# Optimization experiments

Hardware: AMD Instinct MI355X
Metric: run time of the kernel (lower is better)

## Reference

```python
import jax, jax.numpy as jnp
import numpy as np

# model geometry (matches init_kwargs cfg)
D = 768        # D_EMB
PATCH = 16
T = 8192
N = T // PATCH # 512 patch tokens
H = 12         # heads
HD = D // H    # 64 head dim
NL = 6         # layers
DFF = 4 * D
B = 8
LN_EPS = 1e-5


def setup_inputs() -> dict:
    key = jax.random.key(0)
    ks = iter(jax.random.split(key, 32))
    def g(shape, scale=0.02):
        return jax.random.normal(next(ks), shape, jnp.float32) * scale
    return dict(
        x=jax.random.normal(next(ks), (B, T), jnp.float32),
        pp_w=g((D, PATCH)), pp_b=jnp.zeros((D,), jnp.float32),
        pe=g((N, D)),
        ln1_g=jnp.ones((NL, D), jnp.float32), ln1_b=jnp.zeros((NL, D), jnp.float32),
        qkv_w=g((NL, 3 * D, D)), out_w=g((NL, D, D)),
        ln2_g=jnp.ones((NL, D), jnp.float32), ln2_b=jnp.zeros((NL, D), jnp.float32),
        fc1_w=g((NL, DFF, D)), fc2_w=g((NL, D, DFF)),
        lnf_g=jnp.ones((D,), jnp.float32), lnf_b=jnp.zeros((D,), jnp.float32),
        h1_w=g((D // 2, D)), h1_b=jnp.zeros((D // 2,), jnp.float32),
        h2_w=g((2, D // 2)), h2_b=jnp.zeros((2,), jnp.float32),
    )


def _ln(x, g, b):
    m = x.mean(-1, keepdims=True)
    v = ((x - m) ** 2).mean(-1, keepdims=True)
    return (x - m) / jnp.sqrt(v + LN_EPS) * g + b


def reference(x, pp_w, pp_b, pe, ln1_g, ln1_b, qkv_w, out_w,
              ln2_g, ln2_b, fc1_w, fc2_w, lnf_g, lnf_b,
              h1_w, h1_b, h2_w, h2_b):
    Bx = x.shape[0]
    # patch embed: [B, N, PATCH] @ W^T + b -> [B, N, D]
    z = jnp.einsum('bnp,dp->bnd', x[:, :N * PATCH].reshape(Bx, N, PATCH), pp_w) + pp_b
    z = z + pe  # positional embedding (arange indexes whole table)
    mask = jnp.tril(jnp.ones((N, N), dtype=bool))
    for i in range(NL):
        # --- attention (manual causal softmax, dropout=eval/no-op) ---
        h = _ln(z, ln1_g[i], ln1_b[i])
        qkv = jnp.einsum('bnd,ed->bne', h, qkv_w[i])            # [B,N,3D]
        qkv = qkv.reshape(Bx, N, 3, H, HD).transpose(2, 0, 3, 1, 4)
        q, k, v = qkv[0], qkv[1], qkv[2]                         # [B,H,N,HD]
        s = jnp.einsum('bhld,bhmd->bhlm', q, k) / np.sqrt(HD)
        s = jnp.where(mask, s, -jnp.inf)
        a = jax.nn.softmax(s, axis=-1)
        o = jnp.einsum('bhlm,bhmd->bhld', a, v)
        o = o.transpose(0, 2, 1, 3).reshape(Bx, N, D)
        z = z + jnp.einsum('bnd,ed->bne', o, out_w[i])
        # --- FFN (exact gelu, matching F.gelu default) ---
        h = _ln(z, ln2_g[i], ln2_b[i])
        f = jax.nn.gelu(jnp.einsum('bnd,fd->bnf', h, fc1_w[i]), approximate=False)
        z = z + jnp.einsum('bnf,df->bnd', f, fc2_w[i])
    enc = _ln(z, lnf_g, lnf_b).mean(axis=1)                      # [B, D]
    y = jax.nn.relu(enc @ h1_w.T + h1_b)
    return y @ h2_w.T + h2_b                                     # [B, 2]
```

## Files before the change

kernel.cpp:

```cpp
#include <hip/hip_runtime.h>
#include <hip/hip_bf16.h>
#include <math.h>

#define D_EMB 768
#define NPATCH 16
#define NTOK 512
#define NHEAD 12
#define HDIM 64
#define NLAYER 6
#define DFF 3072
#define BATCH 8
#define MTOK (BATCH * NTOK)

typedef __attribute__((ext_vector_type(8))) short bf16x8;
typedef __attribute__((ext_vector_type(4))) float f32x4;

__device__ __forceinline__ float bf2f(ushort s) {
    unsigned u = ((unsigned)s) << 16;
    return __builtin_bit_cast(float, u);
}
__device__ __forceinline__ ushort f2bf(float f) {
    unsigned u = __builtin_bit_cast(unsigned, f);
    unsigned r = (u + 0x7FFFu + ((u >> 16) & 1u)) >> 16;
    return (ushort)r;
}

__global__ __launch_bounds__(256)
void f2bf4_kernel(const float* __restrict__ s0, ushort* __restrict__ d0, int n0,
                  const float* __restrict__ s1, ushort* __restrict__ d1, int n1,
                  const float* __restrict__ s2, ushort* __restrict__ d2, int n2,
                  const float* __restrict__ s3, ushort* __restrict__ d3, int n3)
{
    int i = blockIdx.x * 256 + threadIdx.x;
    const float* s; ushort* d; int off;
    if (i < n0)                { s = s0; d = d0; off = i; }
    else if (i < n0 + n1)      { s = s1; d = d1; off = i - n0; }
    else if (i < n0 + n1 + n2) { s = s2; d = d2; off = i - n0 - n1; }
    else if (i < n0 + n1 + n2 + n3) { s = s3; d = d3; off = i - n0 - n1 - n2; }
    else return;
    float4 v = *(const float4*)(s + (size_t)off * 4);
    ushort4 o;
    o.x = f2bf(v.x); o.y = f2bf(v.y); o.z = f2bf(v.z); o.w = f2bf(v.w);
    *(ushort4*)(d + (size_t)off * 4) = o;
}

__global__ __launch_bounds__(256)
void patch_embed_kernel(const float* __restrict__ x, const float* __restrict__ pw,
                        const float* __restrict__ pb, const float* __restrict__ pe,
                        float* __restrict__ z)
{
    int bn = blockIdx.x;
    int b = bn >> 9, n = bn & 511;
    __shared__ float xs[NPATCH];
    int t = threadIdx.x;
    if (t < NPATCH) xs[t] = x[(size_t)b * 8192 + n * NPATCH + t];
    __syncthreads();
    for (int d = t; d < D_EMB; d += 256) {
        float acc = pb[d] + pe[(size_t)n * D_EMB + d];
        const float* w = pw + (size_t)d * NPATCH;
        #pragma unroll
        for (int p = 0; p < NPATCH; ++p) acc += xs[p] * w[p];
        z[(size_t)bn * D_EMB + d] = acc;
    }
}

__device__ __forceinline__ float block_reduce_sum_256(float v)
{
    __shared__ float lds[4];
    #pragma unroll
    for (int o = 32; o > 0; o >>= 1) v += __shfl_xor(v, o);
    int lane = threadIdx.x & 63, wid = threadIdx.x >> 6;
    __syncthreads();
    if (lane == 0) lds[wid] = v;
    __syncthreads();
    return lds[0] + lds[1] + lds[2] + lds[3];
}

__device__ __forceinline__ void store_val(float* p, float v)  { *p = v; }
__device__ __forceinline__ void store_val(ushort* p, float v) { *p = f2bf(v); }

template<typename OT>
__global__ __launch_bounds__(256)
void ln_kernel(const float* __restrict__ x, const float* __restrict__ g,
               const float* __restrict__ bta, OT* __restrict__ y)
{
    int row = blockIdx.x;
    const float* xr = x + (size_t)row * D_EMB;
    int t = threadIdx.x;
    float vals[3];
    float s = 0.f;
    #pragma unroll
    for (int i = 0; i < 3; ++i) { vals[i] = xr[t + i * 256]; s += vals[i]; }
    float mean = block_reduce_sum_256(s) * (1.0f / D_EMB);
    float ss = 0.f;
    #pragma unroll
    for (int i = 0; i < 3; ++i) { float d = vals[i] - mean; ss += d * d; }
    float var = block_reduce_sum_256(ss) * (1.0f / D_EMB);
    float rstd = rsqrtf(var + 1e-5f);
    #pragma unroll
    for (int i = 0; i < 3; ++i) {
        int d = t + i * 256;
        store_val(y + (size_t)row * D_EMB + d, (vals[i] - mean) * rstd * g[d] + bta[d]);
    }
}

#define STAGE64(buf, k0)                                                           \
    {                                                                              \
        _Pragma("unroll")                                                          \
        for (int j = 0; j < 2; ++j) {                                              \
            int row = j * 32 + srow;                                               \
            int lcol = pcol ^ (row & 7);                                           \
            const ushort* sa = Ab + (size_t)(bm + row) * lda + (k0) + (lcol << 3); \
            __builtin_amdgcn_global_load_lds(                                      \
                (const __attribute__((address_space(1))) unsigned int*)sa,         \
                (__attribute__((address_space(3))) unsigned int*)&As[buf][row * 64 + (pcol << 3)], \
                16, 0, 0);                                                         \
        }                                                                          \
        _Pragma("unroll")                                                          \
        for (int j = 0; j < 4; ++j) {                                              \
            int row = j * 32 + srow;                                               \
            int lcol = pcol ^ (row & 7);                                           \
            const ushort* sb = Wb + (size_t)(bn + row) * lda + (k0) + (lcol << 3); \
            __builtin_amdgcn_global_load_lds(                                      \
                (const __attribute__((address_space(1))) unsigned int*)sb,         \
                (__attribute__((address_space(3))) unsigned int*)&Bs[buf][row * 64 + (pcol << 3)], \
                16, 0, 0);                                                         \
        }                                                                          \
    }

#define COMPUTE64(buf)                                                             \
    {                                                                              \
        _Pragma("unroll")                                                          \
        for (int kk = 0; kk < 64; kk += 32) {                                      \
            int c = (kk >> 3) + lg;                                                \
            bf16x8 a[4], b[2];                                                     \
            _Pragma("unroll")                                                      \
            for (int m = 0; m < 4; ++m) {                                          \
                int row = m * 16 + lr;                                             \
                a[m] = *(const bf16x8*)(&As[buf][row * 64 + ((c ^ (row & 7)) << 3)]); \
            }                                                                      \
            _Pragma("unroll")                                                      \
            for (int n = 0; n < 2; ++n) {                                          \
                int row = w * 32 + n * 16 + lr;                                    \
                b[n] = *(const bf16x8*)(&Bs[buf][row * 64 + ((c ^ (row & 7)) << 3)]); \
            }                                                                      \
            _Pragma("unroll")                                                      \
            for (int m = 0; m < 4; ++m) {                                          \
                _Pragma("unroll")                                                  \
                for (int n = 0; n < 2; ++n)                                        \
                    acc[m][n] = __builtin_amdgcn_mfma_f32_16x16x32_bf16(a[m], b[n], acc[m][n], 0, 0, 0); \
            }                                                                      \
        }                                                                          \
    }

template<int EPI, typename OT, bool SPLITK>
__global__ __launch_bounds__(256)
void mfma_gemm(const ushort* __restrict__ A,
               const ushort* __restrict__ W,
               OT* __restrict__ C,
               const float* __restrict__ res,
               int N, int K, int lda)
{
    __shared__ ushort As[2][64 * 64];
    __shared__ ushort Bs[2][128 * 64];

    int gx = gridDim.x, gy = gridDim.y;
    int bx = blockIdx.x, by = blockIdx.y;
    int bz = SPLITK ? blockIdx.z : 0;
    if ((gy & 7) == 0) {
        int flat = bx + gx * (by + gy * bz);
        int xcd = flat & 7, j = flat >> 3;
        int ry = gy >> 3;
        by = xcd * ry + (j % ry);
        int rem = j / ry;
        bx = rem % gx;
        bz = rem / gx;
    }
    int bm = by * 64, bn = bx * 128;

    const ushort* Ab = A + (size_t)bz * K;
    const ushort* Wb = W + (size_t)bz * K;
    OT* Cb = C + (SPLITK ? (size_t)bz * ((size_t)gy * 64) * N : 0);

    int tid = threadIdx.x;
    int w = tid >> 6, l = tid & 63;
    int lr = l & 15, lg = l >> 4;
    f32x4 acc[4][2] = {};

    int srow = w * 8 + (l >> 3);
    int pcol = l & 7;

    const int nk = K >> 6;
    STAGE64(0, 0);
    __syncthreads();
    int cur = 0;
    for (int t = 0; t < nk; ++t) {
        if (t + 1 < nk) STAGE64(cur ^ 1, (t + 1) << 6);
        COMPUTE64(cur);
        __syncthreads();
        cur ^= 1;
    }

    int r0 = lg * 4;
    #pragma unroll
    for (int m = 0; m < 4; ++m) {
        #pragma unroll
        for (int n = 0; n < 2; ++n) {
            #pragma unroll
            for (int j = 0; j < 4; ++j) {
                int gm = bm + m * 16 + r0 + j;
                int gn = bn + w * 32 + n * 16 + lr;
                float v = acc[m][n][j];
                if (EPI == 1) v = 0.5f * v * (1.0f + erff(v * 0.70710678118654752f));
                if (EPI == 2) v += res[(size_t)gm * N + gn];
                store_val(Cb + (size_t)gm * N + gn, v);
            }
        }
    }
}

__global__ __launch_bounds__(256)
void splitk_reduce(const float* __restrict__ p, float* __restrict__ z, int n4)
{
    int i = blockIdx.x * 256 + threadIdx.x;
    if (i >= n4) return;
    float4 a = ((const float4*)p)[i];
    float4 b = ((const float4*)p)[i + (size_t)n4];
    float4 c = ((float4*)z)[i];
    c.x += a.x + b.x; c.y += a.y + b.y; c.z += a.z + b.z; c.w += a.w + b.w;
    ((float4*)z)[i] = c;
}

__global__ __launch_bounds__(256)
void attn_mfma_kernel(const ushort* __restrict__ qkv, ushort* __restrict__ o)
{
    int w = threadIdx.x >> 6, l = threadIdx.x & 63;
    int qt = blockIdx.x * 4 + w;
    int h = blockIdx.y, b = blockIdx.z;
    int q0 = qt * 16;
    int lr = l & 15, lg = l >> 4;

    const size_t rs = 3 * D_EMB;
    const ushort* qbase = qkv + ((size_t)(b * NTOK)) * rs + h * HDIM;
    const ushort* kbase = qbase + D_EMB;
    const ushort* vbase = qbase + 2 * D_EMB;

    bf16x8 qf[2];
    qf[0] = *(const bf16x8*)(qbase + (size_t)(q0 + lr) * rs + lg * 8);
    qf[1] = *(const bf16x8*)(qbase + (size_t)(q0 + lr) * rs + 32 + lg * 8);

    f32x4 oacc[4] = {};
    float m_j[4], l_j[4];
    #pragma unroll
    for (int j = 0; j < 4; ++j) { m_j[j] = -1e30f; l_j[j] = 0.f; }

    __shared__ ushort P_lds[4][16][40];

    int ntiles = q0 / 32 + 1;
    for (int mt = 0; mt < ntiles; ++mt) {
        int m0 = mt * 32;
        f32x4 s[2] = {};
        #pragma unroll
        for (int kb = 0; kb < 2; ++kb) {
            const ushort* kr = kbase + (size_t)(m0 + kb * 16 + lr) * rs;
            bf16x8 k0 = *(const bf16x8*)(kr + lg * 8);
            bf16x8 k1 = *(const bf16x8*)(kr + 32 + lg * 8);
            s[kb] = __builtin_amdgcn_mfma_f32_16x16x32_bf16(qf[0], k0, s[kb], 0, 0, 0);
            s[kb] = __builtin_amdgcn_mfma_f32_16x16x32_bf16(qf[1], k1, s[kb], 0, 0, 0);
        }
        bool partial = (m0 + 31 > q0);
        float p[2][4], mx[4];
        #pragma unroll
        for (int j = 0; j < 4; ++j) {
            int qr = q0 + lg * 4 + j;
            float s0 = s[0][j] * 0.125f;
            float s1 = s[1][j] * 0.125f;
            if (partial) {
                if (m0 + lr > qr)      s0 = -1e30f;
                if (m0 + 16 + lr > qr) s1 = -1e30f;
            }
            p[0][j] = s0; p[1][j] = s1;
            float mm = fmaxf(s0, s1);
            mm = fmaxf(mm, __shfl_xor(mm, 1));
            mm = fmaxf(mm, __shfl_xor(mm, 2));
            mm = fmaxf(mm, __shfl_xor(mm, 4));
            mm = fmaxf(mm, __shfl_xor(mm, 8));
            mx[j] = mm;
        }
        #pragma unroll
        for (int j = 0; j < 4; ++j) {
            float mnew = fmaxf(m_j[j], mx[j]);
            float scale = __expf(m_j[j] - mnew);
            float p0 = __expf(p[0][j] - mnew);
            float p1 = __expf(p[1][j] - mnew);
            p[0][j] = p0; p[1][j] = p1;
            float rsum = p0 + p1;
            rsum += __shfl_xor(rsum, 1);
            rsum += __shfl_xor(rsum, 2);
            rsum += __shfl_xor(rsum, 4);
            rsum += __shfl_xor(rsum, 8);
            l_j[j] = l_j[j] * scale + rsum;
            m_j[j] = mnew;
            #pragma unroll
            for (int i = 0; i < 4; ++i) oacc[i][j] *= scale;
        }
        #pragma unroll
        for (int kb = 0; kb < 2; ++kb)
            #pragma unroll
            for (int j = 0; j < 4; ++j)
                P_lds[w][lg * 4 + j][kb * 16 + lr] = f2bf(p[kb][j]);
        asm volatile("s_waitcnt lgkmcnt(0)" ::: "memory");
        bf16x8 pa = *(const bf16x8*)(&P_lds[w][lr][lg * 8]);
        #pragma unroll
        for (int i = 0; i < 4; ++i) {
            bf16x8 vf;
            const ushort* vp = vbase + (size_t)(m0 + lg * 8) * rs + i * 16 + lr;
            #pragma unroll
            for (int j = 0; j < 8; ++j) vf[j] = (short)vp[(size_t)j * rs];
            oacc[i] = __builtin_amdgcn_mfma_f32_16x16x32_bf16(pa, vf, oacc[i], 0, 0, 0);
        }
    }
    #pragma unroll
    for (int i = 0; i < 4; ++i) {
        #pragma unroll
        for (int j = 0; j < 4; ++j) {
            int qr = q0 + lg * 4 + j;
            int d  = i * 16 + lr;
            float v = oacc[i][j] / l_j[j];
            o[((size_t)(b * NTOK + qr)) * D_EMB + h * HDIM + d] = f2bf(v);
        }
    }
}

__global__ void mean_kernel(const float* __restrict__ x, float* __restrict__ enc)
{
    int b = blockIdx.x; int d = threadIdx.x;
    float s = 0.f;
    for (int n = 0; n < NTOK; ++n) s += x[((size_t)(b * NTOK + n)) * D_EMB + d];
    enc[b * D_EMB + d] = s * (1.0f / NTOK);
}

__global__ void head1_kernel(const float* __restrict__ enc, const float* __restrict__ w,
                             const float* __restrict__ bias, float* __restrict__ r)
{
    int b = blockIdx.x; int j = threadIdx.x;
    float acc = bias[j];
    const float* e = enc + b * D_EMB;
    const float* wr = w + (size_t)j * D_EMB;
    for (int k = 0; k < D_EMB; ++k) acc += e[k] * wr[k];
    r[b * 384 + j] = fmaxf(acc, 0.f);
}

__global__ void head2_kernel(const float* __restrict__ r, const float* __restrict__ w,
                             const float* __restrict__ bias, float* __restrict__ out)
{
    int idx = threadIdx.x;
    if (idx >= 16) return;
    int b = idx >> 1, j = idx & 1;
    float acc = bias[j];
    for (int k = 0; k < 384; ++k) acc += r[b * 384 + k] * w[j * 384 + k];
    out[b * 2 + j] = acc;
}

extern "C" void kernel_launch(void* const* d_in, const int* in_sizes, int n_in,
                              void* d_out, int out_size, void* d_ws, size_t ws_size,
                              hipStream_t stream)
{
    const float* x     = (const float*)d_in[0];
    const float* pp_w  = (const float*)d_in[1];
    const float* pp_b  = (const float*)d_in[2];
    const float* pe    = (const float*)d_in[3];
    const float* ln1_g = (const float*)d_in[4];
    const float* ln1_b = (const float*)d_in[5];
    const float* qkv_w = (const float*)d_in[6];
    const float* out_w = (const float*)d_in[7];
    const float* ln2_g = (const float*)d_in[8];
    const float* ln2_b = (const float*)d_in[9];
    const float* fc1_w = (const float*)d_in[10];
    const float* fc2_w = (const float*)d_in[11];
    const float* lnf_g = (const float*)d_in[12];
    const float* lnf_b = (const float*)d_in[13];
    const float* h1_w  = (const float*)d_in[14];
    const float* h1_b  = (const float*)d_in[15];
    const float* h2_w  = (const float*)d_in[16];
    const float* h2_b  = (const float*)d_in[17];
    float* out = (float*)d_out;

    char* p = (char*)d_ws;
    float*  z      = (float*)p;  p += (size_t)MTOK * D_EMB * 4;
    ushort* big_bf = (ushort*)p; p += (size_t)MTOK * DFF * 2;
    ushort* h_bf   = (ushort*)p; p += (size_t)MTOK * D_EMB * 2;
    ushort* wq_bf  = (ushort*)p; p += (size_t)3 * D_EMB * D_EMB * 2;
    ushort* wo_bf  = (ushort*)p; p += (size_t)D_EMB * D_EMB * 2;
    ushort* wf1_bf = (ushort*)p; p += (size_t)DFF * D_EMB * 2;
    ushort* wf2_bf = (ushort*)p; p += (size_t)D_EMB * DFF * 2;
    float*  pbuf   = (float*)p;  p += (size_t)2 * MTOK * D_EMB * 4;
    float*  enc    = (float*)p;  p += BATCH * D_EMB * 4;
    float*  r1     = (float*)p;  p += BATCH * 384 * 4;
    float*  lnf_out = (float*)big_bf;

    patch_embed_kernel<<<MTOK, 256, 0, stream>>>(x, pp_w, pp_b, pe, z);

    const int nq = 3 * D_EMB * D_EMB, no = D_EMB * D_EMB, nf = DFF * D_EMB;
    const int n4q = nq / 4, n4o = no / 4, n4f = nf / 4;
    const int cvt_blocks = (n4q + n4o + 2 * n4f + 255) / 256;
    const int n4red = MTOK * D_EMB / 4;

    for (int i = 0; i < NLAYER; ++i) {
        f2bf4_kernel<<<cvt_blocks, 256, 0, stream>>>(
            qkv_w + (size_t)i * nq, wq_bf,  n4q,
            out_w + (size_t)i * no, wo_bf,  n4o,
            fc1_w + (size_t)i * nf, wf1_bf, n4f,
            fc2_w + (size_t)i * nf, wf2_bf, n4f);

        ln_kernel<ushort><<<MTOK, 256, 0, stream>>>(z, ln1_g + i * D_EMB, ln1_b + i * D_EMB, h_bf);

        dim3 gq((3 * D_EMB) / 128, MTOK / 64);
        mfma_gemm<0, ushort, false><<<gq, 256, 0, stream>>>(h_bf, wq_bf, big_bf, nullptr,
                                                            3 * D_EMB, D_EMB, D_EMB);

        dim3 ga(NTOK / 64, NHEAD, BATCH);
        attn_mfma_kernel<<<ga, 256, 0, stream>>>(big_bf, h_bf);

        dim3 gp(D_EMB / 128, MTOK / 64);
        mfma_gemm<2, float, false><<<gp, 256, 0, stream>>>(h_bf, wo_bf, z, z,
                                                           D_EMB, D_EMB, D_EMB);

        ln_kernel<ushort><<<MTOK, 256, 0, stream>>>(z, ln2_g + i * D_EMB, ln2_b + i * D_EMB, h_bf);

        dim3 g1(DFF / 128, MTOK / 64);
        mfma_gemm<1, ushort, false><<<g1, 256, 0, stream>>>(h_bf, wf1_bf, big_bf, nullptr,
                                                            DFF, D_EMB, D_EMB);

        dim3 g2(D_EMB / 128, MTOK / 64, 2);
        mfma_gemm<0, float, true><<<g2, 256, 0, stream>>>(big_bf, wf2_bf, pbuf, nullptr,
                                                          D_EMB, DFF / 2, DFF);
        splitk_reduce<<<(n4red + 255) / 256, 256, 0, stream>>>(pbuf, z, n4red);
    }

    ln_kernel<float><<<MTOK, 256, 0, stream>>>(z, lnf_g, lnf_b, lnf_out);
    mean_kernel<<<BATCH, D_EMB, 0, stream>>>(lnf_out, enc);
    head1_kernel<<<BATCH, 384, 0, stream>>>(enc, h1_w, h1_b, r1);
    head2_kernel<<<1, 64, 0, stream>>>(r1, h2_w, h2_b, out);
}
```

Baseline: 1.110 ms.

## Triple-buffer GEMM pipeline, stage attention V via LDS, fuse split-K reduce with LayerNorm

Moves the GEMM from double to triple buffering, with vmcnt-based waits and a single barrier per K-step so loads run two tiles ahead of the MFMAs. The attention kernel now stages each V tile into LDS with async global-to-LDS loads instead of doing strided global reads per element. The split-K reduction is merged with the next layer's LayerNorm (or the final LN), which removes a kernel launch and one full pass over z. The trade-offs are more shared memory per GEMM block, which can lower occupancy, and hand-written waitcnt counts that must match the exact number of issued loads.

```diff
diff --git a/kernel.cpp b/kernel.cpp
--- a/kernel.cpp
+++ b/kernel.cpp
@@ -91,6 +91,40 @@
     float s = 0.f;
     #pragma unroll
     for (int i = 0; i < 3; ++i) { vals[i] = xr[t + i * 256]; s += vals[i]; }
+    float mean = block_reduce_sum_256(s) * (1.0f / D_EMB);
+    float ss = 0.f;
+    #pragma unroll
+    for (int i = 0; i < 3; ++i) { float d = vals[i] - mean; ss += d * d; }
+    float var = block_reduce_sum_256(ss) * (1.0f / D_EMB);
+    float rstd = rsqrtf(var + 1e-5f);
+    #pragma unroll
+    for (int i = 0; i < 3; ++i) {
+        int d = t + i * 256;
+        store_val(y + (size_t)row * D_EMB + d, (vals[i] - mean) * rstd * g[d] + bta[d]);
+    }
+}
+
+template<typename OT>
+__global__ __launch_bounds__(256)
+void reduce_ln_kernel(const float* __restrict__ pbuf, float* __restrict__ z,
+                      const float* __restrict__ g, const float* __restrict__ bta,
+                      OT* __restrict__ y)
+{
+    int row = blockIdx.x;
+    int t = threadIdx.x;
+    const float* p0 = pbuf + (size_t)row * D_EMB;
+    const float* p1 = pbuf + (size_t)MTOK * D_EMB + (size_t)row * D_EMB;
+    float* zr = z + (size_t)row * D_EMB;
+    float vals[3];
+    float s = 0.f;
+    #pragma unroll
+    for (int i = 0; i < 3; ++i) {
+        int d = t + i * 256;
+        float v = zr[d] + p0[d] + p1[d];
+        vals[i] = v;
+        zr[d] = v;
+        s += v;
+    }
     float mean = block_reduce_sum_256(s) * (1.0f / D_EMB);
     float ss = 0.f;
     #pragma unroll
@@ -131,8 +165,8 @@
 #define COMPUTE64(buf)                                                             \
     {                                                                              \
         _Pragma("unroll")                                                          \
-        for (int kk = 0; kk < 64; kk += 32) {                                      \
-            int c = (kk >> 3) + lg;                                                \
+        for (int kk = 0; kk < 2; ++kk) {                                           \
+            int c = kk * 4 + lg;                                                   \
             bf16x8 a[4], b[2];                                                     \
             _Pragma("unroll")                                                      \
             for (int m = 0; m < 4; ++m) {                                          \
@@ -155,14 +189,12 @@
 
 template<int EPI, typename OT, bool SPLITK>
 __global__ __launch_bounds__(256)
-void mfma_gemm(const ushort* __restrict__ A,
-               const ushort* __restrict__ W,
-               OT* __restrict__ C,
-               const float* __restrict__ res,
+void mfma_gemm(const ushort* __restrict__ A, const ushort* __restrict__ W,
+               OT* __restrict__ C, const float* __restrict__ res,
                int N, int K, int lda)
 {
-    __shared__ ushort As[2][64 * 64];
-    __shared__ ushort Bs[2][128 * 64];
+    __shared__ ushort As[3][64 * 64];
+    __shared__ ushort Bs[3][128 * 64];
 
     int gx = gridDim.x, gy = gridDim.y;
     int bx = blockIdx.x, by = blockIdx.y;
@@ -192,13 +224,16 @@
 
     const int nk = K >> 6;
     STAGE64(0, 0);
-    __syncthreads();
-    int cur = 0;
+    STAGE64(1, 64);
     for (int t = 0; t < nk; ++t) {
-        if (t + 1 < nk) STAGE64(cur ^ 1, (t + 1) << 6);
-        COMPUTE64(cur);
-        __syncthreads();
-        cur ^= 1;
+        if (t < nk - 1) { asm volatile("s_waitcnt vmcnt(6)" ::: "memory"); }
+        else            { asm volatile("s_waitcnt vmcnt(0)" ::: "memory"); }
+        __builtin_amdgcn_s_barrier();
+        if (t + 2 < nk) {
+            int nb = (t + 2) % 3;
+            STAGE64(nb, (t + 2) << 6);
+        }
+        COMPUTE64(t % 3);
     }
 
     int r0 = lg * 4;
@@ -220,18 +255,6 @@
 }
 
 __global__ __launch_bounds__(256)
-void splitk_reduce(const float* __restrict__ p, float* __restrict__ z, int n4)
-{
-    int i = blockIdx.x * 256 + threadIdx.x;
-    if (i >= n4) return;
-    float4 a = ((const float4*)p)[i];
-    float4 b = ((const float4*)p)[i + (size_t)n4];
-    float4 c = ((float4*)z)[i];
-    c.x += a.x + b.x; c.y += a.y + b.y; c.z += a.z + b.z; c.w += a.w + b.w;
-    ((float4*)z)[i] = c;
-}
-
-__global__ __launch_bounds__(256)
 void attn_mfma_kernel(const ushort* __restrict__ qkv, ushort* __restrict__ o)
 {
     int w = threadIdx.x >> 6, l = threadIdx.x & 63;
@@ -254,11 +277,22 @@
     #pragma unroll
     for (int j = 0; j < 4; ++j) { m_j[j] = -1e30f; l_j[j] = 0.f; }
 
+    __shared__ ushort V_lds[4][32 * 64];
     __shared__ ushort P_lds[4][16][40];
 
     int ntiles = q0 / 32 + 1;
     for (int mt = 0; mt < ntiles; ++mt) {
         int m0 = mt * 32;
+        #pragma unroll
+        for (int is = 0; is < 4; ++is) {
+            int row = is * 8 + (l >> 3);
+            int colel = ((l & 7) * 8) ^ (is * 16);
+            const ushort* sv = vbase + (size_t)(m0 + row) * rs + colel;
+            __builtin_amdgcn_global_load_lds(
+                (const __attribute__((address_space(1))) unsigned int*)sv,
+                (__attribute__((address_space(3))) unsigned int*)&V_lds[w][is * 512 + l * 8],
+                16, 0, 0);
+        }
         f32x4 s[2] = {};
         #pragma unroll
         for (int kb = 0; kb < 2; ++kb) {
@@ -311,12 +345,13 @@
                 P_lds[w][lg * 4 + j][kb * 16 + lr] = f2bf(p[kb][j]);
         asm volatile("s_waitcnt lgkmcnt(0)" ::: "memory");
         bf16x8 pa = *(const bf16x8*)(&P_lds[w][lr][lg * 8]);
+        asm volatile("s_waitcnt vmcnt(0)" ::: "memory");
         #pragma unroll
         for (int i = 0; i < 4; ++i) {
             bf16x8 vf;
-            const ushort* vp = vbase + (size_t)(m0 + lg * 8) * rs + i * 16 + lr;
             #pragma unroll
-            for (int j = 0; j < 8; ++j) vf[j] = (short)vp[(size_t)j * rs];
+            for (int j = 0; j < 8; ++j)
+                vf[j] = (short)V_lds[w][(lg * 8 + j) * 64 + ((i * 16 + lr) ^ (lg * 16))];
             oacc[i] = __builtin_amdgcn_mfma_f32_16x16x32_bf16(pa, vf, oacc[i], 0, 0, 0);
         }
     }
@@ -404,7 +439,8 @@
     const int nq = 3 * D_EMB * D_EMB, no = D_EMB * D_EMB, nf = DFF * D_EMB;
     const int n4q = nq / 4, n4o = no / 4, n4f = nf / 4;
     const int cvt_blocks = (n4q + n4o + 2 * n4f + 255) / 256;
-    const int n4red = MTOK * D_EMB / 4;
+
+    ln_kernel<ushort><<<MTOK, 256, 0, stream>>>(z, ln1_g, ln1_b, h_bf);
 
     for (int i = 0; i < NLAYER; ++i) {
         f2bf4_kernel<<<cvt_blocks, 256, 0, stream>>>(
@@ -413,8 +449,6 @@
             fc1_w + (size_t)i * nf, wf1_bf, n4f,
             fc2_w + (size_t)i * nf, wf2_bf, n4f);
 
-        ln_kernel<ushort><<<MTOK, 256, 0, stream>>>(z, ln1_g + i * D_EMB, ln1_b + i * D_EMB, h_bf);
-
         dim3 gq((3 * D_EMB) / 128, MTOK / 64);
         mfma_gemm<0, ushort, false><<<gq, 256, 0, stream>>>(h_bf, wq_bf, big_bf, nullptr,
                                                             3 * D_EMB, D_EMB, D_EMB);
@@ -435,10 +469,16 @@
         dim3 g2(D_EMB / 128, MTOK / 64, 2);
         mfma_gemm<0, float, true><<<g2, 256, 0, stream>>>(big_bf, wf2_bf, pbuf, nullptr,
                                                           D_EMB, DFF / 2, DFF);
-        splitk_reduce<<<(n4red + 255) / 256, 256, 0, stream>>>(pbuf, z, n4red);
-    }
-
-    ln_kernel<float><<<MTOK, 256, 0, stream>>>(z, lnf_g, lnf_b, lnf_out);
+
+        if (i < NLAYER - 1) {
+            reduce_ln_kernel<ushort><<<MTOK, 256, 0, stream>>>(
+                pbuf, z, ln1_g + (i + 1) * D_EMB, ln1_b + (i + 1) * D_EMB, h_bf);
+        } else {
+            reduce_ln_kernel<float><<<MTOK, 256, 0, stream>>>(
+                pbuf, z, lnf_g, lnf_b, lnf_out);
+        }
+    }
+
     mean_kernel<<<BATCH, D_EMB, 0, stream>>>(lnf_out, enc);
     head1_kernel<<<BATCH, 384, 0, stream>>>(enc, h1_w, h1_b, r1);
     head2_kernel<<<1, 64, 0, stream>>>(r1, h2_w, h2_b, out);
```

After: 1.299 ms. 17.1% more time.
